# Kernel optimization log

Hardware: AMD Instinct MI355X
Metric: run time of the kernel (lower is better)

The kernel has to match this reference:

```python
import jax, jax.numpy as jnp
import numpy as np

N, E, IN_DIM, HID, HEADS, OUT_DIM, T = 50000, 200000, 32, 64, 4, 32, 3
NEG_SLOPE = 0.2  # PyG GATv2Conv default


def setup_inputs() -> dict:
    key = jax.random.key(0)
    ks = jax.random.split(key, 16)
    s = 0.1
    return {
        "feat": jax.random.normal(ks[0], (N, IN_DIM), jnp.float32),
        "W_in": jax.random.normal(ks[1], (IN_DIM, HID), jnp.float32) * s,
        "b_in": jnp.zeros((HID,), jnp.float32),
        "Wl": jax.random.normal(ks[2], (2 * HID, HEADS * HID), jnp.float32) * s,
        "bl": jnp.zeros((HEADS * HID,), jnp.float32),
        "Wr": jax.random.normal(ks[3], (2 * HID, HEADS * HID), jnp.float32) * s,
        "br": jnp.zeros((HEADS * HID,), jnp.float32),
        "att": jax.random.normal(ks[4], (HEADS, HID), jnp.float32) * s,
        "b_conv": jnp.zeros((HEADS * HID,), jnp.float32),
        "Wg": jax.random.normal(ks[5], (HID, OUT_DIM), jnp.float32) * s,
        "bg": jnp.zeros((OUT_DIM,), jnp.float32),
        "edge_index": jax.random.randint(ks[6], (2, E), 0, N, jnp.int32),
        "node_mask": jax.random.randint(ks[7], (N,), 0, T + 1, jnp.int32),
        "current_state": jax.random.randint(ks[8], (N,), 0, 2, jnp.int32),
    }


def reference(feat, W_in, b_in, Wl, bl, Wr, br, att, b_conv, Wg, bg,
              edge_index, node_mask, current_state):
    # add self loops (GATv2Conv add_self_loops=True)
    loops = jnp.arange(N, dtype=edge_index.dtype)
    src = jnp.concatenate([edge_index[0], loops])  # [E+N]
    dst = jnp.concatenate([edge_index[1], loops])

    h0 = feat @ W_in + b_in  # [N, HID]
    bias_sum = b_conv.reshape(HEADS, HID).sum(0)  # heads are summed after bias add

    def step(h, i):
        active = node_mask > i  # [N] bool: nodes updated at this step
        x = jnp.concatenate([h, h0], axis=-1)  # [N, 2*HID]
        xl = (x @ Wl + bl).reshape(N, HEADS, HID)  # source transform
        xr = (x @ Wr + br).reshape(N, HEADS, HID)  # target transform
        e_act = active[src] & active[dst]  # edge alive iff both endpoints active
        s = jax.nn.leaky_relu(xl[src] + xr[dst], NEG_SLOPE)  # [E+N, H, C]
        score = jnp.einsum('ehc,hc->eh', s, att)  # [E+N, H]
        score = jnp.where(e_act[:, None], score, -1e30)
        smax = jax.lax.stop_gradient(
            jax.ops.segment_max(score, dst, num_segments=N))  # [N, H]
        ex = jnp.exp(score - smax[dst]) * e_act[:, None].astype(score.dtype)
        denom = jax.ops.segment_sum(ex, dst, num_segments=N)  # [N, H]
        alpha = ex / jnp.maximum(denom[dst], 1e-16)  # segment softmax per dst
        msg = alpha[:, :, None] * xl[src]  # [E+N, H, C]
        agg = jax.ops.segment_sum(msg, dst, num_segments=N)  # [N, H, C]
        out = jnp.tanh(agg.sum(1) + bias_sum)  # sum over heads, then Tanh
        return jnp.where(active[:, None], out, h), None

    h, _ = jax.lax.scan(step, h0, jnp.arange(T))
    # original returns g_embed(h[current_state]); fixed-shape variant: mask rows
    out = (h @ Wg + bg) * (current_state[:, None] > 0).astype(h.dtype)
    return out
```

## Files before the change

kernel.cpp:

```cpp
#include <hip/hip_runtime.h>
#include <hip/hip_bf16.h>

#define NN      50000
#define EE      200000
#define IN_DIM  32
#define HID     64
#define HEADS   4
#define OUTD    32
#define TSTEPS  3

typedef unsigned short bf16_t;
typedef __attribute__((ext_vector_type(8))) short  short8;
typedef __attribute__((ext_vector_type(4))) float  floatx4;

__device__ __forceinline__ float b2f(bf16_t u) {
    union { unsigned int i; float f; } v; v.i = ((unsigned int)u) << 16; return v.f;
}
__device__ __forceinline__ bf16_t f2b(float f) {
    union { float f; unsigned int i; } v; v.f = f;
    unsigned int r = v.i + 0x7FFF + ((v.i >> 16) & 1);
    return (bf16_t)(r >> 16);
}

#define DPP_ADD(x, ctrl) ((x) + __int_as_float(                                 \
        __builtin_amdgcn_update_dpp(0, __float_as_int(x), (ctrl), 0xF, 0xF, true)))

#define H0_BLOCKS ((NN + 63) / 64)
#define NB_NODE   ((NN + 255) / 256)
#define NBC       (NB_NODE * 4)
#define EB        ((EE + 1023) / 1024)

__global__ __launch_bounds__(256) void k_setup(
        const void* W_in, const void* b_in, const void* att, const void* bconv,
        const void* Wg, const void* bg,
        const void* Wl_raw, const void* Wr_raw, const void* bl_raw, const void* br_raw,
        const void* feat_raw, const int* __restrict__ nmask,
        const int* __restrict__ e_src, const int* __restrict__ e_dst,
        float* attf, float* bcf, float* Wgf, float* bgf,
        bf16_t* __restrict__ Wt, bf16_t* __restrict__ WtS, float* __restrict__ bb,
        int* __restrict__ deg4, int* __restrict__ flag, int* __restrict__ bcount,
        bf16_t* __restrict__ h0, bf16_t* __restrict__ h) {
    __shared__ int bad;
    __shared__ float Ws[IN_DIM * HID];
    __shared__ float bs[HID];
    __shared__ int wcnt[4][4];
    int t = threadIdx.x, bid = blockIdx.x;
    if (t == 0) bad = 0;
    __syncthreads();
    {
        const bf16_t* p = (const bf16_t*)W_in;
        int mybad = 0;
        for (int i = t; i < IN_DIM * HID; i += 256) {
            float v = b2f(p[i]);
            if (v != v || fabsf(v) > 100.f) mybad = 1;
        }
        if (mybad) atomicOr(&bad, 1);
    }
    __syncthreads();
    int f = bad ? 0 : 1;
    if (bid == 0 && t == 0) *flag = f;

    if (bid < 256) {
        int i = bid * 256 + t;
        int n = i >> 7, k = i & 127;
        const void* W = (n < 256) ? Wl_raw : Wr_raw;
        int nn = (n < 256) ? n : n - 256;
        float v = f ? b2f(((const bf16_t*)W)[k * 256 + nn])
                    : ((const float*)W)[k * 256 + nn];
        Wt[n * 128 + k] = f2b(v);
        if (k < 64) {
            float v2 = f ? b2f(((const bf16_t*)W)[(k + 64) * 256 + nn])
                         : ((const float*)W)[(k + 64) * 256 + nn];
            WtS[n * 64 + k] = f2b(v + v2);
        }
        if (k == 0) {
            const void* b = (n < 256) ? bl_raw : br_raw;
            bb[n] = f ? b2f(((const bf16_t*)b)[nn]) : ((const float*)b)[nn];
        }
    } else if (bid < 267) {
        int i = (bid - 256) * 256 + t;
        const void* src; float* dst; int off;
        if      (i < 256)  { src = att;   dst = attf; off = i; }
        else if (i < 512)  { src = bconv; dst = bcf;  off = i - 256; }
        else if (i < 2560) { src = Wg;    dst = Wgf;  off = i - 512; }
        else if (i < 2592) { src = bg;    dst = bgf;  off = i - 2560; }
        else return;
        dst[off] = f ? b2f(((const bf16_t*)src)[off]) : ((const float*)src)[off];
    } else if (bid < 267 + NB_NODE) {
        int nb = bid - 267;
        int i = nb * 256 + t;
        bool valid = i < NN;
        int wid = t >> 6, lane = t & 63;
        int v = 0;
        if (valid) { int m = nmask[i]; v = m < 0 ? 0 : (m > 3 ? 3 : m); }
#pragma unroll
        for (int b = 0; b < 4; b++) {
            unsigned long long mm = __ballot(valid && v == b);
            if (lane == 0) wcnt[wid][b] = __popcll(mm);
        }
        __syncthreads();
        if (t < 4)
            bcount[nb * 4 + t] = wcnt[0][t] + wcnt[1][t] + wcnt[2][t] + wcnt[3][t];
    } else if (bid < 267 + NB_NODE + EB) {
        int nb = bid - 267 - NB_NODE;
        int i = (nb * 256 + t) * 4;
        if (i + 3 < EE) {
            int4 dv = *(const int4*)(e_dst + i);
            int4 sv = *(const int4*)(e_src + i);
            int m0 = nmask[sv.x]; m0 = m0 < 0 ? 0 : (m0 > 3 ? 3 : m0);
            int m1 = nmask[sv.y]; m1 = m1 < 0 ? 0 : (m1 > 3 ? 3 : m1);
            int m2 = nmask[sv.z]; m2 = m2 < 0 ? 0 : (m2 > 3 ? 3 : m2);
            int m3 = nmask[sv.w]; m3 = m3 < 0 ? 0 : (m3 > 3 ? 3 : m3);
            atomicAdd(&deg4[dv.x * 4 + m0], 1);
            atomicAdd(&deg4[dv.y * 4 + m1], 1);
            atomicAdd(&deg4[dv.z * 4 + m2], 1);
            atomicAdd(&deg4[dv.w * 4 + m3], 1);
        } else {
            for (; i < EE; i++) {
                int s = e_src[i];
                int m = nmask[s]; m = m < 0 ? 0 : (m > 3 ? 3 : m);
                atomicAdd(&deg4[e_dst[i] * 4 + m], 1);
            }
        }
    } else {
        for (int i = t; i < IN_DIM * HID; i += 256)
            Ws[i] = f ? b2f(((const bf16_t*)W_in)[i]) : ((const float*)W_in)[i];
        if (t < HID)
            bs[t] = f ? b2f(((const bf16_t*)b_in)[t]) : ((const float*)b_in)[t];
        __syncthreads();
        int nb = bid - (267 + NB_NODE + EB);
        int wid = t >> 6, c = t & 63;
#pragma unroll
        for (int g = 0; g < 16; g++) {
            int node = (nb * 16 + g) * 4 + wid;
            if (node >= NN) break;
            float acc = bs[c];
            if (f) {
                const short8* fr8 = (const short8*)((const bf16_t*)feat_raw
                                                    + (size_t)node * IN_DIM);
#pragma unroll
                for (int j = 0; j < 4; j++) {
                    short8 fv = fr8[j];
#pragma unroll
                    for (int k = 0; k < 8; k++)
                        acc += b2f((bf16_t)fv[k]) * Ws[(j * 8 + k) * HID + c];
                }
            } else {
                const float4* fr4 = (const float4*)((const float*)feat_raw
                                                    + (size_t)node * IN_DIM);
#pragma unroll
                for (int j = 0; j < 8; j++) {
                    float4 fv = fr4[j];
                    acc += fv.x * Ws[(j * 4 + 0) * HID + c];
                    acc += fv.y * Ws[(j * 4 + 1) * HID + c];
                    acc += fv.z * Ws[(j * 4 + 2) * HID + c];
                    acc += fv.w * Ws[(j * 4 + 3) * HID + c];
                }
            }
            bf16_t o = f2b(acc);
            h0[(size_t)node * HID + c] = o;
            h [(size_t)node * HID + c] = o;
        }
    }
}

__global__ __launch_bounds__(256) void k_scan(const int* __restrict__ deg4,
                                              int* __restrict__ cur4,
                                              int* __restrict__ rend4,
                                              const int* __restrict__ bcount,
                                              int* __restrict__ mbuf,
                                              int n, int nch) {
    __shared__ int sc[256];
    __shared__ int spre[256];
    __shared__ int cb[4];
    int t = threadIdx.x, bid = blockIdx.x;

    if (bid == 0) {
        if (t < 4) cb[t] = 0;
        __syncthreads();
        for (int i = t; i < NBC; i += 256) atomicAdd(&cb[i & 3], bcount[i]);
        __syncthreads();
        if (t == 0) {
            int c1 = cb[1], c2 = cb[2], c3 = cb[3];
            mbuf[7] = 0;
            mbuf[6] = c3;
            mbuf[5] = c3 + c2;
            mbuf[4] = c3 + c2 + c1;
            mbuf[8] = c3 + c2 + c1;
            mbuf[9] = c3 + c2;
            mbuf[10] = c3;
        }
    }

    const int4* d4 = (const int4*)deg4;
    int base = bid * 1024;
    int pre = 0;
    for (int i = t; i < base; i += 256) {
        int4 q = d4[i];
        pre += q.x + q.y + q.z + q.w;
    }
    spre[t] = pre; __syncthreads();
    for (int off = 128; off > 0; off >>= 1) {
        if (t < off) spre[t] += spre[t + off];
        __syncthreads();
    }
    int bpref = spre[0];

    int4 dd[4]; int tot[4]; int s = 0;
#pragma unroll
    for (int j = 0; j < 4; j++) {
        int i = base + t * 4 + j;
        if (i < n) dd[j] = d4[i];
        else { dd[j].x = 0; dd[j].y = 0; dd[j].z = 0; dd[j].w = 0; }
        tot[j] = dd[j].x + dd[j].y + dd[j].z + dd[j].w;
        s += tot[j];
    }
    sc[t] = s; __syncthreads();
    for (int off = 1; off < 256; off <<= 1) {
        int add = (t >= off) ? sc[t - off] : 0;
        __syncthreads();
        sc[t] += add;
        __syncthreads();
    }
    int run = sc[t] - s + bpref;
#pragma unroll
    for (int j = 0; j < 4; j++) {
        int i = base + t * 4 + j;
        if (i < n) {
            int c3 = run;
            int c2 = c3 + dd[j].w;
            int c1 = c2 + dd[j].z;
            int c0 = c1 + dd[j].y;
            int4 cu; cu.x = c0; cu.y = c1; cu.z = c2; cu.w = c3;
            *(int4*)(cur4 + i * 4) = cu;
            int4 re; re.x = c0; re.y = c1; re.z = c2; re.w = run;
            *(int4*)(rend4 + i * 4) = re;
        }
        run += tot[j];
    }
}

__global__ __launch_bounds__(256) void k_scatter_all(const int* __restrict__ src,
                                                     const int* __restrict__ dst,
                                                     int* __restrict__ cur4,
                                                     int* __restrict__ col,
                                                     const int* __restrict__ mask,
                                                     int* __restrict__ mbuf,
                                                     int* __restrict__ order) {
    int t = threadIdx.x, bid = blockIdx.x;
    int i = bid * 256 + t;
    if (i < EE) {
        int sv = src[i];
        int m = mask[sv]; m = m < 0 ? 0 : (m > 3 ? 3 : m);
        int d = dst[i];
        int pos = atomicAdd(&cur4[d * 4 + m], 1);
        col[pos] = sv;
    }
    if (bid < NB_NODE) {
        __shared__ int wcnt[4][4];
        __shared__ int bbase[4];
        int wid = t >> 6, lane = t & 63;
        int ni = bid * 256 + t;
        bool valid = ni < NN;
        int v = 0;
        if (valid) { int m = mask[ni]; v = m < 0 ? 0 : (m > 3 ? 3 : m); }
        int rank = 0;
#pragma unroll
        for (int b = 0; b < 4; b++) {
            unsigned long long mm = __ballot(valid && v == b);
            if (valid && v == b)
                rank = __popcll(mm & ((lane == 0) ? 0ull : (~0ull >> (64 - lane))));
            if (lane == 0) wcnt[wid][b] = __popcll(mm);
        }
        __syncthreads();
        if (t < 4) {
            int tot = wcnt[0][t] + wcnt[1][t] + wcnt[2][t] + wcnt[3][t];
            bbase[t] = atomicAdd(&mbuf[4 + t], tot);
        }
        __syncthreads();
        if (valid) {
            int wpre = 0;
            for (int ww = 0; ww < wid; ww++) wpre += wcnt[ww][v];
            order[bbase[v] + wpre + rank] = ni;
        }
    }
}

__global__ __launch_bounds__(256) void k_gemm0(const bf16_t* __restrict__ h0,
                                               const bf16_t* __restrict__ WtS,
                                               const float* __restrict__ bb,
                                               bf16_t* __restrict__ xl,
                                               bf16_t* __restrict__ xr,
                                               const int* __restrict__ order,
                                               const int* __restrict__ mbuf) {
    int count = mbuf[8];
    int mbase = blockIdx.x * 64;
    if (mbase >= count) return;

    __shared__ bf16_t smem[64 * 72 + 128 * 72];
    bf16_t* As = smem;
    bf16_t* Bs = smem + 64 * 72;
    bf16_t* Cs = smem;

    int t = threadIdx.x;
    int nbase = blockIdx.y * 128;

    {
        int ln = t >> 2, lq = t & 3;
        int idx = mbase + ln;
        int node = (idx < count) ? order[idx] : -1;
        ulonglong2 z; z.x = 0; z.y = 0;
        ulonglong2 v0 = z, v1 = z;
        if (node >= 0) {
            v0 = *(const ulonglong2*)(h0 + (size_t)node * HID + lq * 16);
            v1 = *(const ulonglong2*)(h0 + (size_t)node * HID + lq * 16 + 8);
        }
        *(ulonglong2*)(&As[ln * 72 + lq * 16]) = v0;
        *(ulonglong2*)(&As[ln * 72 + lq * 16 + 8]) = v1;
    }
    {
        int n = t >> 1, kc = (t & 1) * 32;
        const bf16_t* srcp = WtS + (size_t)(nbase + n) * 64 + kc;
        bf16_t* dstp = &Bs[n * 72 + kc];
        *(ulonglong2*)(dstp)      = *(const ulonglong2*)(srcp);
        *(ulonglong2*)(dstp + 8)  = *(const ulonglong2*)(srcp + 8);
        *(ulonglong2*)(dstp + 16) = *(const ulonglong2*)(srcp + 16);
        *(ulonglong2*)(dstp + 24) = *(const ulonglong2*)(srcp + 24);
    }
    __syncthreads();

    int wv = t >> 6, lane = t & 63, mrow = lane & 15, quad = lane >> 4;
    floatx4 acc[8];
#pragma unroll
    for (int nf = 0; nf < 8; nf++) acc[nf] = (floatx4){0.f, 0.f, 0.f, 0.f};
#pragma unroll
    for (int kq = 0; kq < 2; kq++) {
        short8 a = *(const short8*)(&As[(wv * 16 + mrow) * 72 + kq * 32 + quad * 8]);
#pragma unroll
        for (int nf = 0; nf < 8; nf++) {
            short8 b = *(const short8*)(&Bs[(nf * 16 + mrow) * 72 + kq * 32 + quad * 8]);
            acc[nf] = __builtin_amdgcn_mfma_f32_16x16x32_bf16(a, b, acc[nf], 0, 0, 0);
        }
    }
    __syncthreads();

#pragma unroll
    for (int nf = 0; nf < 8; nf++) {
        float bv = bb[nbase + nf * 16 + mrow];
#pragma unroll
        for (int r = 0; r < 4; r++) {
            int m = wv * 16 + quad * 4 + r;
            Cs[m * 136 + nf * 16 + mrow] = f2b(acc[nf][r] + bv);
        }
    }
    __syncthreads();

    bf16_t* outp = (blockIdx.y < 2) ? xl : xr;
    int cc = (blockIdx.y & 1) * 128;
#pragma unroll
    for (int i = 0; i < 4; i++) {
        int c = t + i * 256;
        int m = c >> 4, kc = (c & 15) * 8;
        int idx = mbase + m;
        if (idx < count) {
            int node = order[idx];
            *(ulonglong2*)(outp + (size_t)node * 256 + cc + kc) =
                *(const ulonglong2*)(&Cs[m * 136 + kc]);
        }
    }
}

__global__ __launch_bounds__(256) void k_gemm_mfma(const bf16_t* __restrict__ h,
                                                   const bf16_t* __restrict__ h0,
                                                   const bf16_t* __restrict__ Wt,
                                                   const float* __restrict__ bb,
                                                   bf16_t* __restrict__ xl,
                                                   bf16_t* __restrict__ xr,
                                                   const int* __restrict__ order,
                                                   const int* __restrict__ mbuf,
                                                   int step) {
    int count = mbuf[8 + step];
    int mbase = blockIdx.x * 64;
    if (mbase >= count) return;

    __shared__ bf16_t smem[64 * 136 + 128 * 136];
    bf16_t* As = smem;
    bf16_t* Bs = smem + 64 * 136;
    bf16_t* Cs = smem;

    int t = threadIdx.x;
    int nbase = blockIdx.y * 128;

    {
        int ln = t >> 2, lq = t & 3;
        int idx = mbase + ln;
        int node = (idx < count) ? order[idx] : -1;
        ulonglong2 z; z.x = 0; z.y = 0;
#pragma unroll
        for (int j = 0; j < 2; j++) {
            int chunk = lq + j * 4;
            ulonglong2 vh = z, vh0 = z;
            if (node >= 0) {
                vh  = *(const ulonglong2*)(h  + (size_t)node * HID + chunk * 8);
                vh0 = *(const ulonglong2*)(h0 + (size_t)node * HID + chunk * 8);
            }
            *(ulonglong2*)(&As[ln * 136 + chunk * 8]) = vh;
            *(ulonglong2*)(&As[ln * 136 + 64 + chunk * 8]) = vh0;
        }
    }
#pragma unroll
    for (int i = 0; i < 8; i++) {
        int c = t + i * 256;
        int n = c >> 4, kc = (c & 15) * 8;
        *(ulonglong2*)(&Bs[n * 136 + kc]) =
            *(const ulonglong2*)(Wt + (size_t)(nbase + n) * 128 + kc);
    }
    __syncthreads();

    int wv = t >> 6, lane = t & 63, mrow = lane & 15, quad = lane >> 4;
    floatx4 acc[8];
#pragma unroll
    for (int nf = 0; nf < 8; nf++) acc[nf] = (floatx4){0.f, 0.f, 0.f, 0.f};
#pragma unroll
    for (int kq = 0; kq < 4; kq++) {
        short8 a = *(const short8*)(&As[(wv * 16 + mrow) * 136 + kq * 32 + quad * 8]);
#pragma unroll
        for (int nf = 0; nf < 8; nf++) {
            short8 b = *(const short8*)(&Bs[(nf * 16 + mrow) * 136 + kq * 32 + quad * 8]);
            acc[nf] = __builtin_amdgcn_mfma_f32_16x16x32_bf16(a, b, acc[nf], 0, 0, 0);
        }
    }
    __syncthreads();

#pragma unroll
    for (int nf = 0; nf < 8; nf++) {
        float bv = bb[nbase + nf * 16 + mrow];
#pragma unroll
        for (int r = 0; r < 4; r++) {
            int m = wv * 16 + quad * 4 + r;
            Cs[m * 136 + nf * 16 + mrow] = f2b(acc[nf][r] + bv);
        }
    }
    __syncthreads();

    bf16_t* outp = (blockIdx.y < 2) ? xl : xr;
    int cc = (blockIdx.y & 1) * 128;
#pragma unroll
    for (int i = 0; i < 4; i++) {
        int c = t + i * 256;
        int m = c >> 4, kc = (c & 15) * 8;
        int idx = mbase + m;
        if (idx < count) {
            int node = order[idx];
            *(ulonglong2*)(outp + (size_t)node * 256 + cc + kc) =
                *(const ulonglong2*)(&Cs[m * 136 + kc]);
        }
    }
}

template<int STEP>
__global__ __launch_bounds__(256) void k_agg(bf16_t* __restrict__ h,
                                             const bf16_t* __restrict__ xl,
                                             const bf16_t* __restrict__ xr,
                                             const float* __restrict__ att,
                                             const float* __restrict__ b_conv,
                                             const int* __restrict__ rend4,
                                             const int* __restrict__ col,
                                             const int* __restrict__ order,
                                             const int* __restrict__ mbuf) {
    int count = mbuf[8 + STEP];
    int t = threadIdx.x;
    int wid = t >> 6, lane = t & 63;
    int half = lane >> 5, s = lane & 31;

    float4 avL = *(const float4*)(att + s * 8);
    float4 avH = *(const float4*)(att + s * 8 + 4);
    avL.x *= 1.44269504f; avL.y *= 1.44269504f; avL.z *= 1.44269504f; avL.w *= 1.44269504f;
    avH.x *= 1.44269504f; avH.y *= 1.44269504f; avH.z *= 1.44269504f; avH.w *= 1.44269504f;
    float4 bcL = *(const float4*)(b_conv + s * 8);
    float4 bcH = *(const float4*)(b_conv + s * 8 + 4);

    const int pstride = gridDim.x * 8;
    for (int p0 = (blockIdx.x * 4 + wid) * 2; p0 < count; p0 += pstride) {
        int myidx = p0 + half;
        bool valid = myidx < count;
        int node = order[valid ? myidx : count - 1];

        int4 re = *(const int4*)(rend4 + node * 4);
        int e0 = re.w;
        int e1 = (STEP == 0) ? re.x : (STEP == 1) ? re.y : re.z;
        int nl = e1 - e0;
        int nother = __shfl_xor(nl, 32, 64);
        int nmax = nl > nother ? nl : nother;

        short8 us  = *(const short8*)(xl + (size_t)node * 256 + s * 8);
        short8 xru = *(const short8*)(xr + (size_t)node * 256 + s * 8);
        float xr0 = b2f((bf16_t)xru[0]), xr1 = b2f((bf16_t)xru[1]);
        float xr2 = b2f((bf16_t)xru[2]), xr3 = b2f((bf16_t)xru[3]);
        float xr4 = b2f((bf16_t)xru[4]), xr5 = b2f((bf16_t)xru[5]);
        float xr6 = b2f((bf16_t)xru[6]), xr7 = b2f((bf16_t)xru[7]);

        float l = 0.f;
        float c0 = 0.f, c1 = 0.f, c2 = 0.f, c3 = 0.f;
        float c4 = 0.f, c5 = 0.f, c6 = 0.f, c7 = 0.f;

        auto body = [&](short8 xu, bool live) {
            float x0 = b2f((bf16_t)xu[0]), x1 = b2f((bf16_t)xu[1]);
            float x2 = b2f((bf16_t)xu[2]), x3 = b2f((bf16_t)xu[3]);
            float x4 = b2f((bf16_t)xu[4]), x5 = b2f((bf16_t)xu[5]);
            float x6 = b2f((bf16_t)xu[6]), x7 = b2f((bf16_t)xu[7]);
            float v0 = x0 + xr0; v0 = fmaxf(v0, 0.2f * v0);
            float v1 = x1 + xr1; v1 = fmaxf(v1, 0.2f * v1);
            float v2 = x2 + xr2; v2 = fmaxf(v2, 0.2f * v2);
            float v3 = x3 + xr3; v3 = fmaxf(v3, 0.2f * v3);
            float v4 = x4 + xr4; v4 = fmaxf(v4, 0.2f * v4);
            float v5 = x5 + xr5; v5 = fmaxf(v5, 0.2f * v5);
            float v6 = x6 + xr6; v6 = fmaxf(v6, 0.2f * v6);
            float v7 = x7 + xr7; v7 = fmaxf(v7, 0.2f * v7);
            float part = avL.x * v0 + avL.y * v1 + avL.z * v2 + avL.w * v3
                       + avH.x * v4 + avH.y * v5 + avH.z * v6 + avH.w * v7;
            part = DPP_ADD(part, 0xB1);
            part = DPP_ADD(part, 0x4E);
            part = DPP_ADD(part, 0x141);
            float p = live ? exp2f(part) : 0.f;
            l += p;
            c0 += p * x0; c1 += p * x1; c2 += p * x2; c3 += p * x3;
            c4 += p * x4; c5 += p * x5; c6 += p * x6; c7 += p * x7;
        };

        body(us, valid);
        for (int j = 0; j < nmax; j += 4) {
            int e = e0 + j;
            int q0 = col[e], q1 = col[e + 1], q2 = col[e + 2], q3 = col[e + 3];
            short8 r0 = *(const short8*)(xl + (size_t)q0 * 256 + s * 8);
            short8 r1 = *(const short8*)(xl + (size_t)q1 * 256 + s * 8);
            short8 r2 = *(const short8*)(xl + (size_t)q2 * 256 + s * 8);
            short8 r3 = *(const short8*)(xl + (size_t)q3 * 256 + s * 8);
            body(r0, j + 0 < nl);
            body(r1, j + 1 < nl);
            body(r2, j + 2 < nl);
            body(r3, j + 3 < nl);
        }

        float inv = __builtin_amdgcn_rcpf(l);
        float t0 = c0 * inv + bcL.x, t1 = c1 * inv + bcL.y;
        float t2 = c2 * inv + bcL.z, t3 = c3 * inv + bcL.w;
        float t4 = c4 * inv + bcH.x, t5 = c5 * inv + bcH.y;
        float t6 = c6 * inv + bcH.z, t7 = c7 * inv + bcH.w;
        t0 += __shfl_xor(t0, 8, 64); t0 += __shfl_xor(t0, 16, 64);
        t1 += __shfl_xor(t1, 8, 64); t1 += __shfl_xor(t1, 16, 64);
        t2 += __shfl_xor(t2, 8, 64); t2 += __shfl_xor(t2, 16, 64);
        t3 += __shfl_xor(t3, 8, 64); t3 += __shfl_xor(t3, 16, 64);
        t4 += __shfl_xor(t4, 8, 64); t4 += __shfl_xor(t4, 16, 64);
        t5 += __shfl_xor(t5, 8, 64); t5 += __shfl_xor(t5, 16, 64);
        t6 += __shfl_xor(t6, 8, 64); t6 += __shfl_xor(t6, 16, 64);
        t7 += __shfl_xor(t7, 8, 64); t7 += __shfl_xor(t7, 16, 64);
        if (valid && s < 8) {
            short8 o;
            o[0] = (short)f2b(tanhf(t0)); o[1] = (short)f2b(tanhf(t1));
            o[2] = (short)f2b(tanhf(t2)); o[3] = (short)f2b(tanhf(t3));
            o[4] = (short)f2b(tanhf(t4)); o[5] = (short)f2b(tanhf(t5));
            o[6] = (short)f2b(tanhf(t6)); o[7] = (short)f2b(tanhf(t7));
            *(short8*)(h + (size_t)node * HID + s * 8) = o;
        }
    }
}

__global__ __launch_bounds__(256) void k_out(const bf16_t* __restrict__ h,
                                             const float* __restrict__ Wg,
                                             const float* __restrict__ bg,
                                             const int* __restrict__ cs,
                                             void* __restrict__ out,
                                             const int* __restrict__ flag) {
    __shared__ float Ws[HID * OUTD];
    __shared__ float bs[OUTD];
    int t = threadIdx.x;
    for (int i = t; i < HID * OUTD; i += 256) Ws[i] = Wg[i];
    if (t < OUTD) bs[t] = bg[t];
    __syncthreads();
    int g0 = t >> 5, c = t & 31;
    int fl = *flag;
#pragma unroll
    for (int g = 0; g < 4; g++) {
        int node = blockIdx.x * 32 + g * 8 + g0;
        if (node >= NN) break;
        float res = 0.f;
        if (cs[node] > 0) {
            const short8* hr8 = (const short8*)(h + (size_t)node * HID);
            float acc = bs[c];
#pragma unroll
            for (int j = 0; j < 8; j++) {
                short8 hv = hr8[j];
#pragma unroll
                for (int k = 0; k < 8; k++)
                    acc += b2f((bf16_t)hv[k]) * Ws[(j * 8 + k) * OUTD + c];
            }
            res = acc;
        }
        size_t idx = (size_t)node * OUTD + c;
        if (fl) ((bf16_t*)out)[idx] = f2b(res);
        else    ((float*)out)[idx]  = res;
    }
}

static inline size_t alignup(size_t x) { return (x + 255) & ~(size_t)255; }

extern "C" void kernel_launch(void* const* d_in, const int* in_sizes, int n_in,
                              void* d_out, int out_size, void* d_ws, size_t ws_size,
                              hipStream_t stream) {
    const void* feat_raw  = d_in[0];
    const void* W_in_raw  = d_in[1];
    const void* b_in_raw  = d_in[2];
    const void* Wl_raw    = d_in[3];
    const void* bl_raw    = d_in[4];
    const void* Wr_raw    = d_in[5];
    const void* br_raw    = d_in[6];
    const void* att_raw   = d_in[7];
    const void* bconv_raw = d_in[8];
    const void* Wg_raw    = d_in[9];
    const void* bg_raw    = d_in[10];
    const int* edge       = (const int*)d_in[11];
    const int* nmask      = (const int*)d_in[12];
    const int* cstate     = (const int*)d_in[13];

    const int* e_src = edge;
    const int* e_dst = edge + EE;

    const size_t SZ_HB   = alignup((size_t)NN * HID * sizeof(bf16_t));
    const size_t SZ_X    = alignup((size_t)NN * 256 * sizeof(bf16_t));
    const size_t SZ_I4   = alignup((size_t)NN * 4 * sizeof(int));
    const size_t SZ_I    = alignup((size_t)NN * sizeof(int));
    const size_t SZ_COL  = alignup((size_t)EE * sizeof(int));
    const int nch = (NN + 1023) / 1024;
    const size_t SZ_BC   = alignup((size_t)NBC * sizeof(int));
    const size_t SZ_WT   = alignup((size_t)512 * 128 * sizeof(bf16_t));
    const size_t SZ_WTS  = alignup((size_t)512 * 64 * sizeof(bf16_t));
    const size_t SZ_B    = alignup(512 * sizeof(float));
    const size_t SZ_WG   = alignup((size_t)HID * OUTD * sizeof(float));

    char* w = (char*)d_ws;
    bf16_t* h0   = (bf16_t*)w; w += SZ_HB;
    bf16_t* h    = (bf16_t*)w; w += SZ_HB;
    bf16_t* xl   = (bf16_t*)w; w += SZ_X;
    bf16_t* xr   = (bf16_t*)w; w += SZ_X;
    int* deg4    = (int*)w;    w += SZ_I4;
    int* mbuf    = (int*)w;    w += 256;
    int* cur4    = (int*)w;    w += SZ_I4;
    int* rend4   = (int*)w;    w += SZ_I4;
    int* colA    = (int*)w;    w += SZ_COL;
    int* order   = (int*)w;    w += SZ_I;
    int* bcount  = (int*)w;    w += SZ_BC;
    bf16_t* Wt   = (bf16_t*)w; w += SZ_WT;
    bf16_t* WtS  = (bf16_t*)w; w += SZ_WTS;
    float* bb    = (float*)w;  w += SZ_B;
    float* attf  = (float*)w;  w += SZ_B;
    float* bcf   = (float*)w;  w += SZ_B;
    float* Wgf   = (float*)w;  w += SZ_WG;
    float* bgf   = (float*)w;  w += SZ_B;
    int* flag    = (int*)w;    w += 256;
    if ((size_t)(w - (char*)d_ws) > ws_size) return;

    hipMemsetAsync(deg4, 0, SZ_I4 + 256, stream);

    k_setup<<<267 + NB_NODE + EB + H0_BLOCKS, 256, 0, stream>>>(
        W_in_raw, b_in_raw, att_raw, bconv_raw, Wg_raw, bg_raw,
        Wl_raw, Wr_raw, bl_raw, br_raw, feat_raw, nmask, e_src, e_dst,
        attf, bcf, Wgf, bgf, Wt, WtS, bb, deg4, flag, bcount, h0, h);

    k_scan<<<nch, 256, 0, stream>>>(deg4, cur4, rend4, bcount, mbuf, NN, nch);
    k_scatter_all<<<(EE + 255) / 256, 256, 0, stream>>>(e_src, e_dst, cur4, colA,
                                                        nmask, mbuf, order);

    k_gemm0<<<dim3((NN + 63) / 64, 4), 256, 0, stream>>>(h0, WtS, bb, xl, xr, order, mbuf);
    k_agg<0><<<2048, 256, 0, stream>>>(h, xl, xr, attf, bcf, rend4, colA, order, mbuf);

    k_gemm_mfma<<<dim3((NN + 63) / 64, 4), 256, 0, stream>>>(h, h0, Wt, bb, xl, xr,
                                                             order, mbuf, 1);
    k_agg<1><<<2048, 256, 0, stream>>>(h, xl, xr, attf, bcf, rend4, colA, order, mbuf);
    k_gemm_mfma<<<dim3((NN + 63) / 64, 4), 256, 0, stream>>>(h, h0, Wt, bb, xl, xr,
                                                             order, mbuf, 2);
    k_agg<2><<<2048, 256, 0, stream>>>(h, xl, xr, attf, bcf, rend4, colA, order, mbuf);

    k_out<<<(NN + 31) / 32, 256, 0, stream>>>(h, Wgf, bgf, cstate, d_out, flag);
}
```

Baseline: 277.1 us.

## Renumber nodes into mask-sorted order and pack h/h0 contiguously

Nodes are renumbered by their position in the mask-sorted order. Edge columns are rewritten to the new ranks, and h and h0 are packed side by side into one 128-wide row per rank. The GEMM and aggregation kernels then index xl, xr and h directly by rank, so their loads and stores become contiguous instead of going through the order indirection. This costs an extra pack kernel, extra rank and re_p buffers, and a gather through order in the output kernel.

```diff
diff --git a/kernel.cpp b/kernel.cpp
--- a/kernel.cpp
+++ b/kernel.cpp
@@ -29,6 +29,8 @@
 #define NB_NODE   ((NN + 255) / 256)
 #define NBC       (NB_NODE * 4)
 #define EB        ((EE + 1023) / 1024)
+#define PB_COL    ((EE + 1023) / 1024)
+#define PB_HP     ((NN + 63) / 64)
 
 __global__ __launch_bounds__(256) void k_setup(
         const void* W_in, const void* b_in, const void* att, const void* bconv,
@@ -39,7 +41,7 @@
         float* attf, float* bcf, float* Wgf, float* bgf,
         bf16_t* __restrict__ Wt, bf16_t* __restrict__ WtS, float* __restrict__ bb,
         int* __restrict__ deg4, int* __restrict__ flag, int* __restrict__ bcount,
-        bf16_t* __restrict__ h0, bf16_t* __restrict__ h) {
+        bf16_t* __restrict__ h0) {
     __shared__ int bad;
     __shared__ float Ws[IN_DIM * HID];
     __shared__ float bs[HID];
@@ -157,9 +159,7 @@
                     acc += fv.w * Ws[(j * 4 + 3) * HID + c];
                 }
             }
-            bf16_t o = f2b(acc);
-            h0[(size_t)node * HID + c] = o;
-            h [(size_t)node * HID + c] = o;
+            h0[(size_t)node * HID + c] = f2b(acc);
         }
     }
 }
@@ -245,8 +245,11 @@
                                                      int* __restrict__ cur4,
                                                      int* __restrict__ col,
                                                      const int* __restrict__ mask,
+                                                     const int* __restrict__ rend4,
                                                      int* __restrict__ mbuf,
-                                                     int* __restrict__ order) {
+                                                     int* __restrict__ order,
+                                                     int* __restrict__ rank,
+                                                     int* __restrict__ re_p) {
     int t = threadIdx.x, bid = blockIdx.x;
     int i = bid * 256 + t;
     if (i < EE) {
@@ -264,12 +267,12 @@
         bool valid = ni < NN;
         int v = 0;
         if (valid) { int m = mask[ni]; v = m < 0 ? 0 : (m > 3 ? 3 : m); }
-        int rank = 0;
+        int rk = 0;
 #pragma unroll
         for (int b = 0; b < 4; b++) {
             unsigned long long mm = __ballot(valid && v == b);
             if (valid && v == b)
-                rank = __popcll(mm & ((lane == 0) ? 0ull : (~0ull >> (64 - lane))));
+                rk = __popcll(mm & ((lane == 0) ? 0ull : (~0ull >> (64 - lane))));
             if (lane == 0) wcnt[wid][b] = __popcll(mm);
         }
         __syncthreads();
@@ -281,17 +284,50 @@
         if (valid) {
             int wpre = 0;
             for (int ww = 0; ww < wid; ww++) wpre += wcnt[ww][v];
-            order[bbase[v] + wpre + rank] = ni;
-        }
-    }
-}
-
-__global__ __launch_bounds__(256) void k_gemm0(const bf16_t* __restrict__ h0,
+            int pos = bbase[v] + wpre + rk;
+            order[pos] = ni;
+            rank[ni] = pos;
+            *(int4*)(re_p + pos * 4) = *(const int4*)(rend4 + ni * 4);
+        }
+    }
+}
+
+__global__ __launch_bounds__(256) void k_pack(int* __restrict__ col,
+                                              const int* __restrict__ rank,
+                                              const int* __restrict__ order,
+                                              const bf16_t* __restrict__ h0,
+                                              bf16_t* __restrict__ hp) {
+    int t = threadIdx.x, bid = blockIdx.x;
+    if (bid < PB_COL) {
+        int i = (bid * 256 + t) * 4;
+        if (i + 3 < EE) {
+            int4 c = *(const int4*)(col + i);
+            c.x = rank[c.x]; c.y = rank[c.y]; c.z = rank[c.z]; c.w = rank[c.w];
+            *(int4*)(col + i) = c;
+        } else {
+            for (; i < EE; i++) col[i] = rank[col[i]];
+        }
+    } else {
+        int nb = bid - PB_COL;
+        int ln = t >> 2, lq = t & 3;
+        int idx = nb * 64 + ln;
+        if (idx >= NN) return;
+        int node = order[idx];
+        ulonglong2 v0 = *(const ulonglong2*)(h0 + (size_t)node * HID + lq * 16);
+        ulonglong2 v1 = *(const ulonglong2*)(h0 + (size_t)node * HID + lq * 16 + 8);
+        bf16_t* dstp = hp + (size_t)idx * 128;
+        *(ulonglong2*)(dstp + lq * 16)       = v0;
+        *(ulonglong2*)(dstp + lq * 16 + 8)   = v1;
+        *(ulonglong2*)(dstp + 64 + lq * 16)  = v0;
+        *(ulonglong2*)(dstp + 64 + lq * 16 + 8) = v1;
+    }
+}
+
+__global__ __launch_bounds__(256) void k_gemm0(const bf16_t* __restrict__ hp,
                                                const bf16_t* __restrict__ WtS,
                                                const float* __restrict__ bb,
                                                bf16_t* __restrict__ xl,
                                                bf16_t* __restrict__ xr,
-                                               const int* __restrict__ order,
                                                const int* __restrict__ mbuf) {
     int count = mbuf[8];
     int mbase = blockIdx.x * 64;
@@ -308,12 +344,11 @@
     {
         int ln = t >> 2, lq = t & 3;
         int idx = mbase + ln;
-        int node = (idx < count) ? order[idx] : -1;
         ulonglong2 z; z.x = 0; z.y = 0;
         ulonglong2 v0 = z, v1 = z;
-        if (node >= 0) {
-            v0 = *(const ulonglong2*)(h0 + (size_t)node * HID + lq * 16);
-            v1 = *(const ulonglong2*)(h0 + (size_t)node * HID + lq * 16 + 8);
+        if (idx < count) {
+            v0 = *(const ulonglong2*)(hp + (size_t)idx * 128 + lq * 16);
+            v1 = *(const ulonglong2*)(hp + (size_t)idx * 128 + lq * 16 + 8);
         }
         *(ulonglong2*)(&As[ln * 72 + lq * 16]) = v0;
         *(ulonglong2*)(&As[ln * 72 + lq * 16 + 8]) = v1;
@@ -363,20 +398,17 @@
         int m = c >> 4, kc = (c & 15) * 8;
         int idx = mbase + m;
         if (idx < count) {
-            int node = order[idx];
-            *(ulonglong2*)(outp + (size_t)node * 256 + cc + kc) =
+            *(ulonglong2*)(outp + (size_t)idx * 256 + cc + kc) =
                 *(const ulonglong2*)(&Cs[m * 136 + kc]);
         }
     }
 }
 
-__global__ __launch_bounds__(256) void k_gemm_mfma(const bf16_t* __restrict__ h,
-                                                   const bf16_t* __restrict__ h0,
+__global__ __launch_bounds__(256) void k_gemm_mfma(const bf16_t* __restrict__ hp,
                                                    const bf16_t* __restrict__ Wt,
                                                    const float* __restrict__ bb,
                                                    bf16_t* __restrict__ xl,
                                                    bf16_t* __restrict__ xr,
-                                                   const int* __restrict__ order,
                                                    const int* __restrict__ mbuf,
                                                    int step) {
     int count = mbuf[8 + step];
@@ -394,18 +426,16 @@
     {
         int ln = t >> 2, lq = t & 3;
         int idx = mbase + ln;
-        int node = (idx < count) ? order[idx] : -1;
         ulonglong2 z; z.x = 0; z.y = 0;
 #pragma unroll
         for (int j = 0; j < 2; j++) {
-            int chunk = lq + j * 4;
-            ulonglong2 vh = z, vh0 = z;
-            if (node >= 0) {
-                vh  = *(const ulonglong2*)(h  + (size_t)node * HID + chunk * 8);
-                vh0 = *(const ulonglong2*)(h0 + (size_t)node * HID + chunk * 8);
+            ulonglong2 v0 = z, v1 = z;
+            if (idx < count) {
+                v0 = *(const ulonglong2*)(hp + (size_t)idx * 128 + lq * 32 + j * 16);
+                v1 = *(const ulonglong2*)(hp + (size_t)idx * 128 + lq * 32 + j * 16 + 8);
             }
-            *(ulonglong2*)(&As[ln * 136 + chunk * 8]) = vh;
-            *(ulonglong2*)(&As[ln * 136 + 64 + chunk * 8]) = vh0;
+            *(ulonglong2*)(&As[ln * 136 + lq * 32 + j * 16]) = v0;
+            *(ulonglong2*)(&As[ln * 136 + lq * 32 + j * 16 + 8]) = v1;
         }
     }
 #pragma unroll
@@ -451,22 +481,20 @@
         int m = c >> 4, kc = (c & 15) * 8;
         int idx = mbase + m;
         if (idx < count) {
-            int node = order[idx];
-            *(ulonglong2*)(outp + (size_t)node * 256 + cc + kc) =
+            *(ulonglong2*)(outp + (size_t)idx * 256 + cc + kc) =
                 *(const ulonglong2*)(&Cs[m * 136 + kc]);
         }
     }
 }
 
 template<int STEP>
-__global__ __launch_bounds__(256) void k_agg(bf16_t* __restrict__ h,
+__global__ __launch_bounds__(256) void k_agg(bf16_t* __restrict__ hp,
                                              const bf16_t* __restrict__ xl,
                                              const bf16_t* __restrict__ xr,
                                              const float* __restrict__ att,
                                              const float* __restrict__ b_conv,
-                                             const int* __restrict__ rend4,
+                                             const int* __restrict__ re_p,
                                              const int* __restrict__ col,
-                                             const int* __restrict__ order,
                                              const int* __restrict__ mbuf) {
     int count = mbuf[8 + STEP];
     int t = threadIdx.x;
@@ -484,17 +512,17 @@
     for (int p0 = (blockIdx.x * 4 + wid) * 2; p0 < count; p0 += pstride) {
         int myidx = p0 + half;
         bool valid = myidx < count;
-        int node = order[valid ? myidx : count - 1];
-
-        int4 re = *(const int4*)(rend4 + node * 4);
+        int ridx = valid ? myidx : count - 1;
+
+        int4 re = *(const int4*)(re_p + ridx * 4);
         int e0 = re.w;
         int e1 = (STEP == 0) ? re.x : (STEP == 1) ? re.y : re.z;
         int nl = e1 - e0;
         int nother = __shfl_xor(nl, 32, 64);
         int nmax = nl > nother ? nl : nother;
 
-        short8 us  = *(const short8*)(xl + (size_t)node * 256 + s * 8);
-        short8 xru = *(const short8*)(xr + (size_t)node * 256 + s * 8);
+        short8 us  = *(const short8*)(xl + (size_t)ridx * 256 + s * 8);
+        short8 xru = *(const short8*)(xr + (size_t)ridx * 256 + s * 8);
         float xr0 = b2f((bf16_t)xru[0]), xr1 = b2f((bf16_t)xru[1]);
         float xr2 = b2f((bf16_t)xru[2]), xr3 = b2f((bf16_t)xru[3]);
         float xr4 = b2f((bf16_t)xru[4]), xr5 = b2f((bf16_t)xru[5]);
@@ -561,17 +589,20 @@
             o[2] = (short)f2b(tanhf(t2)); o[3] = (short)f2b(tanhf(t3));
             o[4] = (short)f2b(tanhf(t4)); o[5] = (short)f2b(tanhf(t5));
             o[6] = (short)f2b(tanhf(t6)); o[7] = (short)f2b(tanhf(t7));
-            *(short8*)(h + (size_t)node * HID + s * 8) = o;
-        }
-    }
-}
-
-__global__ __launch_bounds__(256) void k_out(const bf16_t* __restrict__ h,
+            *(short8*)(hp + (size_t)ridx * 128 + s * 8) = o;
+        }
+    }
+}
+
+__global__ __launch_bounds__(256) void k_out(const bf16_t* __restrict__ hp,
+                                             const bf16_t* __restrict__ h0,
+                                             const int* __restrict__ order,
                                              const float* __restrict__ Wg,
                                              const float* __restrict__ bg,
                                              const int* __restrict__ cs,
                                              void* __restrict__ out,
-                                             const int* __restrict__ flag) {
+                                             const int* __restrict__ flag,
+                                             const int* __restrict__ mbuf) {
     __shared__ float Ws[HID * OUTD];
     __shared__ float bs[OUTD];
     int t = threadIdx.x;
@@ -580,13 +611,17 @@
     __syncthreads();
     int g0 = t >> 5, c = t & 31;
     int fl = *flag;
+    int c0cnt = mbuf[8];
 #pragma unroll
     for (int g = 0; g < 4; g++) {
-        int node = blockIdx.x * 32 + g * 8 + g0;
-        if (node >= NN) break;
+        int idx = blockIdx.x * 32 + g * 8 + g0;
+        if (idx >= NN) break;
+        int node = order[idx];
         float res = 0.f;
         if (cs[node] > 0) {
-            const short8* hr8 = (const short8*)(h + (size_t)node * HID);
+            const bf16_t* hr = (idx < c0cnt) ? (hp + (size_t)idx * 128)
+                                             : (h0 + (size_t)node * HID);
+            const short8* hr8 = (const short8*)hr;
             float acc = bs[c];
 #pragma unroll
             for (int j = 0; j < 8; j++) {
@@ -597,9 +632,9 @@
             }
             res = acc;
         }
-        size_t idx = (size_t)node * OUTD + c;
-        if (fl) ((bf16_t*)out)[idx] = f2b(res);
-        else    ((float*)out)[idx]  = res;
+        size_t oidx = (size_t)node * OUTD + c;
+        if (fl) ((bf16_t*)out)[oidx] = f2b(res);
+        else    ((float*)out)[oidx]  = res;
     }
 }
 
@@ -627,6 +662,7 @@
     const int* e_dst = edge + EE;
 
     const size_t SZ_HB   = alignup((size_t)NN * HID * sizeof(bf16_t));
+    const size_t SZ_HP   = alignup((size_t)NN * 128 * sizeof(bf16_t));
     const size_t SZ_X    = alignup((size_t)NN * 256 * sizeof(bf16_t));
     const size_t SZ_I4   = alignup((size_t)NN * 4 * sizeof(int));
     const size_t SZ_I    = alignup((size_t)NN * sizeof(int));
@@ -640,15 +676,17 @@
 
     char* w = (char*)d_ws;
     bf16_t* h0   = (bf16_t*)w; w += SZ_HB;
-    bf16_t* h    = (bf16_t*)w; w += SZ_HB;
+    bf16_t* hp   = (bf16_t*)w; w += SZ_HP;
     bf16_t* xl   = (bf16_t*)w; w += SZ_X;
     bf16_t* xr   = (bf16_t*)w; w += SZ_X;
     int* deg4    = (int*)w;    w += SZ_I4;
     int* mbuf    = (int*)w;    w += 256;
     int* cur4    = (int*)w;    w += SZ_I4;
     int* rend4   = (int*)w;    w += SZ_I4;
+    int* re_p    = (int*)w;    w += SZ_I4;
     int* colA    = (int*)w;    w += SZ_COL;
     int* order   = (int*)w;    w += SZ_I;
+    int* rank    = (int*)w;    w += SZ_I;
     int* bcount  = (int*)w;    w += SZ_BC;
     bf16_t* Wt   = (bf16_t*)w; w += SZ_WT;
     bf16_t* WtS  = (bf16_t*)w; w += SZ_WTS;
@@ -665,21 +703,22 @@
     k_setup<<<267 + NB_NODE + EB + H0_BLOCKS, 256, 0, stream>>>(
         W_in_raw, b_in_raw, att_raw, bconv_raw, Wg_raw, bg_raw,
         Wl_raw, Wr_raw, bl_raw, br_raw, feat_raw, nmask, e_src, e_dst,
-        attf, bcf, Wgf, bgf, Wt, WtS, bb, deg4, flag, bcount, h0, h);
+        attf, bcf, Wgf, bgf, Wt, WtS, bb, deg4, flag, bcount, h0);
 
     k_scan<<<nch, 256, 0, stream>>>(deg4, cur4, rend4, bcount, mbuf, NN, nch);
     k_scatter_all<<<(EE + 255) / 256, 256, 0, stream>>>(e_src, e_dst, cur4, colA,
-                                                        nmask, mbuf, order);
-
-    k_gemm0<<<dim3((NN + 63) / 64, 4), 256, 0, stream>>>(h0, WtS, bb, xl, xr, order, mbuf);
-    k_agg<0><<<2048, 256, 0, stream>>>(h, xl, xr, attf, bcf, rend4, colA, order, mbuf);
-
-    k_gemm_mfma<<<dim3((NN + 63) / 64, 4), 256, 0, stream>>>(h, h0, Wt, bb, xl, xr,
-                                                             order, mbuf, 1);
-    k_agg<1><<<2048, 256, 0, stream>>>(h, xl, xr, attf, bcf, rend4, colA, order, mbuf);
-    k_gemm_mfma<<<dim3((NN + 63) / 64, 4), 256, 0, stream>>>(h, h0, Wt, bb, xl, xr,
-                                                             order, mbuf, 2);
-    k_agg<2><<<2048, 256, 0, stream>>>(h, xl, xr, attf, bcf, rend4, colA, order, mbuf);
-
-    k_out<<<(NN + 31) / 32, 256, 0, stream>>>(h, Wgf, bgf, cstate, d_out, flag);
-}
+                                                        nmask, rend4, mbuf,
+                                                        order, rank, re_p);
+    k_pack<<<PB_COL + PB_HP, 256, 0, stream>>>(colA, rank, order, h0, hp);
+
+    k_gemm0<<<dim3((NN + 63) / 64, 4), 256, 0, stream>>>(hp, WtS, bb, xl, xr, mbuf);
+    k_agg<0><<<2048, 256, 0, stream>>>(hp, xl, xr, attf, bcf, re_p, colA, mbuf);
+
+    k_gemm_mfma<<<dim3((NN + 63) / 64, 4), 256, 0, stream>>>(hp, Wt, bb, xl, xr, mbuf, 1);
+    k_agg<1><<<2048, 256, 0, stream>>>(hp, xl, xr, attf, bcf, re_p, colA, mbuf);
+    k_gemm_mfma<<<dim3((NN + 63) / 64, 4), 256, 0, stream>>>(hp, Wt, bb, xl, xr, mbuf, 2);
+    k_agg<2><<<2048, 256, 0, stream>>>(hp, xl, xr, attf, bcf, re_p, colA, mbuf);
+
+    k_out<<<(NN + 31) / 32, 256, 0, stream>>>(hp, h0, order, Wgf, bgf, cstate,
+                                              d_out, flag, mbuf);
+}
```

After: 274.0 us. Within noise of the previous version (-1.1%).
